# Kernel tuning notes

Measured on AMD Instinct MI355X. Metric: run time of the kernel, lower is better.

Reference implementation:

```python
import jax, jax.numpy as jnp
import numpy as np

N_USERS, N_MOVIES, H, E = 100000, 50000, 128, 1000000


def setup_inputs() -> dict:
    key = jax.random.key(0)
    k1, k2, k3, k4, k5, k6 = jax.random.split(key, 6)
    scale1 = 1.0 / np.sqrt(2 * H)  # torch Linear default-ish init scale
    scale2 = 1.0 / np.sqrt(H)
    return {
        "z_user": jax.random.normal(k1, (N_USERS, H), dtype=jnp.float32),
        "z_movie": jax.random.normal(k2, (N_MOVIES, H), dtype=jnp.float32),
        "row": jax.random.randint(k3, (E,), 0, N_USERS, dtype=jnp.int64) if jax.config.jax_enable_x64 else jax.random.randint(k3, (E,), 0, N_USERS, dtype=jnp.int32),
        "col": jax.random.randint(k4, (E,), 0, N_MOVIES, dtype=jnp.int32),
        "W1": jax.random.normal(k5, (H, 2 * H), dtype=jnp.float32) * scale1,
        "b1": jnp.zeros((H,), dtype=jnp.float32),
        "W2": jax.random.normal(k6, (1, H), dtype=jnp.float32) * scale2,
        "b2": jnp.zeros((1,), dtype=jnp.float32),
    }


def reference(z_user, z_movie, row, col, W1, b1, W2, b2):
    zu = z_user[row]            # [E, H] gather
    zm = z_movie[col]           # [E, H] gather
    z = jnp.concatenate([zu, zm], axis=-1)        # [E, 2H]
    h = jax.nn.relu(z @ W1.T + b1)                # [E, H]
    out = h @ W2.T + b2                           # [E, 1]
    return out.reshape(-1)
```

## Files before the change

kernel.cpp:

```cpp
#include <hip/hip_runtime.h>
#include <stdint.h>

typedef __attribute__((ext_vector_type(8))) short bf16x8;
typedef __attribute__((ext_vector_type(8))) char  char8;
typedef __attribute__((ext_vector_type(4))) float f32x4;
typedef __attribute__((ext_vector_type(4))) int   i32x4;

#define SU      (4.5f / 127.0f)
#define INV_SU  (127.0f / 4.5f)

__device__ __forceinline__ unsigned short f2bf(float f) {
    uint32_t u = __builtin_bit_cast(uint32_t, f);
    uint32_t r = (u + 0x7FFFu + ((u >> 16) & 1u)) >> 16;
    return (unsigned short)r;
}

__device__ __forceinline__ float bf2f(unsigned short u) {
    return __builtin_bit_cast(float, (uint32_t)u << 16);
}

__device__ __forceinline__ bf16x8 cvt8(f32x4 a, f32x4 b) {
    bf16x8 v;
#pragma unroll
    for (int i = 0; i < 4; ++i) v[i] = (short)f2bf(a[i]);
#pragma unroll
    for (int i = 0; i < 4; ++i) v[4 + i] = (short)f2bf(b[i]);
    return v;
}

__device__ __forceinline__ unsigned swz256(int n, int kbyte) {
    return ((unsigned)(n * 256 + kbyte)) ^ (unsigned)((n & 7) << 4);
}

__global__ __launch_bounds__(256) void precompute_h1(
    const float* __restrict__ zu, const float* __restrict__ zm,
    const float* __restrict__ W1, const float* __restrict__ b1,
    char* __restrict__ h1u8, char* __restrict__ h1m8,
    int Mu, int Mm, int bu)
{
    __shared__ __align__(16) char Bs[32768];
    const int tid  = threadIdx.x;
    const int wid  = tid >> 6;
    const int lane = tid & 63;
    const int g    = lane >> 4;
    const int lm   = lane & 15;

    const bool isU = (int)blockIdx.x < bu;
    const float* z = isU ? zu : zm;
    char* h1       = isU ? h1u8 : h1m8;
    const int M    = isU ? Mu : Mm;
    const int koff = isU ? 0 : 128;
    const int rbase = (isU ? blockIdx.x : blockIdx.x - bu) * 128 + wid * 32;

#pragma unroll
    for (int it = 0; it < 8; ++it) {
        int c  = it * 256 + tid;
        int n  = c >> 4;
        int kc = c & 15;
        const float* src = W1 + n * 256 + koff + kc * 8;
        f32x4 a = *reinterpret_cast<const f32x4*>(src);
        f32x4 b = *reinterpret_cast<const f32x4*>(src + 4);
        *reinterpret_cast<bf16x8*>(&Bs[swz256(n, kc * 16)]) = cvt8(a, b);
    }
    __syncthreads();

    f32x4 b1q[8];
#pragma unroll
    for (int nt = 0; nt < 8; ++nt) {
        f32x4 t = *reinterpret_cast<const f32x4*>(b1 + nt * 16 + g * 4);
#pragma unroll
        for (int r = 0; r < 4; ++r) b1q[nt][r] = 0.5f * t[r];
    }

    f32x4 acc[2][8];
#pragma unroll
    for (int mt = 0; mt < 2; ++mt)
#pragma unroll
        for (int nt = 0; nt < 8; ++nt) acc[mt][nt] = f32x4{0.f, 0.f, 0.f, 0.f};

#pragma unroll
    for (int ks = 0; ks < 4; ++ks) {
        bf16x8 a[2];
#pragma unroll
        for (int mt = 0; mt < 2; ++mt) {
            int r = rbase + mt * 16 + lm;
            r = r < M ? r : M - 1;
            const float* p = z + (size_t)r * 128 + ks * 32 + g * 8;
            f32x4 x0 = *reinterpret_cast<const f32x4*>(p);
            f32x4 x1 = *reinterpret_cast<const f32x4*>(p + 4);
            a[mt] = cvt8(x0, x1);
        }
        const int kbyte = (ks * 32 + g * 8) * 2;
#pragma unroll
        for (int nt = 0; nt < 8; ++nt) {
            bf16x8 bfr = *reinterpret_cast<const bf16x8*>(&Bs[swz256(nt * 16 + lm, kbyte)]);
#pragma unroll
            for (int mt = 0; mt < 2; ++mt)
                acc[mt][nt] = __builtin_amdgcn_mfma_f32_16x16x32_bf16(
                    bfr, a[mt], acc[mt][nt], 0, 0, 0);
        }
    }

#pragma unroll
    for (int mt = 0; mt < 2; ++mt) {
        const int m = rbase + mt * 16 + lm;
        if (m >= M) continue;
#pragma unroll
        for (int nt = 0; nt < 8; ++nt) {
            uint32_t p = 0;
#pragma unroll
            for (int r = 0; r < 4; ++r) {
                float h  = acc[mt][nt][r] + b1q[nt][r];
                float qf = fmaxf(-127.f, fminf(127.f, __builtin_rintf(h * INV_SU)));
                int   q  = (int)qf;
                p |= (uint32_t)(q & 0xff) << (8 * r);
            }
            *reinterpret_cast<uint32_t*>(h1 + (size_t)m * 128 + nt * 16 + g * 4) = p;
        }
    }
}

__global__ __launch_bounds__(256) void edge_score(
    const char* __restrict__ h1u8, const char* __restrict__ h1m8,
    const int* __restrict__ row, const int* __restrict__ col,
    const float* __restrict__ W2, const float* __restrict__ b2,
    float* __restrict__ out, int nE)
{
    const int tid = blockIdx.x * 256 + threadIdx.x;
    const int g   = tid >> 4;
    const int l   = tid & 15;
    const int e0  = g * 8;
    if (e0 >= nE) return;

    float w2s[8];
    {
        f32x4 c0 = *reinterpret_cast<const f32x4*>(W2 + l * 8);
        f32x4 c1 = *reinterpret_cast<const f32x4*>(W2 + l * 8 + 4);
#pragma unroll
        for (int j = 0; j < 4; ++j) { w2s[j] = c0[j] * SU; w2s[4 + j] = c1[j] * SU; }
    }
    const float b2s = b2[0];

    int ridx[8], cidx[8];
    if (e0 + 8 <= nE) {
        i32x4 r0 = __builtin_nontemporal_load(reinterpret_cast<const i32x4*>(row + e0));
        i32x4 r1 = __builtin_nontemporal_load(reinterpret_cast<const i32x4*>(row + e0 + 4));
        i32x4 c0 = __builtin_nontemporal_load(reinterpret_cast<const i32x4*>(col + e0));
        i32x4 c1 = __builtin_nontemporal_load(reinterpret_cast<const i32x4*>(col + e0 + 4));
#pragma unroll
        for (int j = 0; j < 4; ++j) { ridx[j] = r0[j]; ridx[4 + j] = r1[j]; }
#pragma unroll
        for (int j = 0; j < 4; ++j) { cidx[j] = c0[j]; cidx[4 + j] = c1[j]; }
    } else {
#pragma unroll
        for (int j = 0; j < 8; ++j) {
            int e = e0 + j;
            e = e < nE ? e : nE - 1;
            ridx[j] = row[e];
            cidx[j] = col[e];
        }
    }

    char8 u[8], m[8];
#pragma unroll
    for (int j = 0; j < 8; ++j)
        u[j] = *reinterpret_cast<const char8*>(h1u8 + (size_t)ridx[j] * 128 + l * 8);
#pragma unroll
    for (int j = 0; j < 8; ++j)
        m[j] = *reinterpret_cast<const char8*>(h1m8 + (size_t)cidx[j] * 128 + l * 8);
    __builtin_amdgcn_sched_barrier(0);

    float s[8];
#pragma unroll
    for (int j = 0; j < 8; ++j) {
        float acc = 0.f;
#pragma unroll
        for (int q = 0; q < 8; ++q) {
            int su = (int)u[j][q] + (int)m[j][q];
            su = su > 0 ? su : 0;
            acc = fmaf((float)su, w2s[q], acc);
        }
        acc += __shfl_xor(acc, 1);
        acc += __shfl_xor(acc, 2);
        acc += __shfl_xor(acc, 4);
        acc += __shfl_xor(acc, 8);
        s[j] = acc + b2s;
    }

    float v = 0.f;
#pragma unroll
    for (int j = 0; j < 8; ++j) v = (l == j) ? s[j] : v;
    const int e = e0 + l;
    if (l < 8 && e < nE) __builtin_nontemporal_store(v, out + e);
}

__device__ __forceinline__ unsigned swzB(int n, int kbyte) {
    return ((unsigned)(n * 512 + kbyte)) ^ (unsigned)((n & 7) << 4);
}

__global__ __launch_bounds__(256, 2) void edge_mlp_fallback(
    const float* __restrict__ z_user, const float* __restrict__ z_movie,
    const int* __restrict__ row, const int* __restrict__ col,
    const float* __restrict__ W1, const float* __restrict__ b1,
    const float* __restrict__ W2, const float* __restrict__ b2,
    float* __restrict__ out, int nE, int ntiles)
{
    __shared__ __align__(16) char Bs[65536];
    const int tid  = threadIdx.x;
    const int wid  = tid >> 6;
    const int lane = tid & 63;
    const int g    = lane >> 4;
    const int lm   = lane & 15;

#pragma unroll
    for (int it = 0; it < 16; ++it) {
        int c  = it * 256 + tid;
        int n  = c >> 5;
        int kc = c & 31;
        const float* src = W1 + n * 256 + kc * 8;
        f32x4 a = *reinterpret_cast<const f32x4*>(src);
        f32x4 b = *reinterpret_cast<const f32x4*>(src + 4);
        *reinterpret_cast<bf16x8*>(&Bs[swzB(n, kc * 16)]) = cvt8(a, b);
    }
    __syncthreads();

    float b1v[8], w2v[8];
#pragma unroll
    for (int nt = 0; nt < 8; ++nt) {
        int n = nt * 16 + lm;
        b1v[nt] = b1[n];
        w2v[nt] = W2[n];
    }
    const float b2s = b2[0];

    for (int tile = blockIdx.x; tile < ntiles; tile += gridDim.x) {
        const int ebase = tile * 256 + wid * 64;
        int re[4], ce[4];
#pragma unroll
        for (int mt = 0; mt < 4; ++mt) {
            int e = ebase + mt * 16 + lm;
            e = e < nE ? e : nE - 1;
            re[mt] = row[e];
            ce[mt] = col[e];
        }
        f32x4 acc[4][8];
#pragma unroll
        for (int mt = 0; mt < 4; ++mt)
#pragma unroll
            for (int nt = 0; nt < 8; ++nt) acc[mt][nt] = f32x4{0.f, 0.f, 0.f, 0.f};
#pragma unroll
        for (int half = 0; half < 2; ++half) {
#pragma unroll
            for (int ks = 0; ks < 4; ++ks) {
                bf16x8 a[4];
#pragma unroll
                for (int mt = 0; mt < 4; ++mt) {
                    const float* p = (half ? z_movie + (size_t)ce[mt] * 128
                                           : z_user + (size_t)re[mt] * 128) + ks * 32 + g * 8;
                    f32x4 x0 = *reinterpret_cast<const f32x4*>(p);
                    f32x4 x1 = *reinterpret_cast<const f32x4*>(p + 4);
                    a[mt] = cvt8(x0, x1);
                }
                const int kbyte = (half * 128 + ks * 32 + g * 8) * 2;
#pragma unroll
                for (int nt = 0; nt < 8; ++nt) {
                    bf16x8 bfr = *reinterpret_cast<const bf16x8*>(&Bs[swzB(nt * 16 + lm, kbyte)]);
#pragma unroll
                    for (int mt = 0; mt < 4; ++mt)
                        acc[mt][nt] = __builtin_amdgcn_mfma_f32_16x16x32_bf16(
                            a[mt], bfr, acc[mt][nt], 0, 0, 0);
                }
            }
        }
#pragma unroll
        for (int mt = 0; mt < 4; ++mt) {
#pragma unroll
            for (int r = 0; r < 4; ++r) {
                float s = 0.f;
#pragma unroll
                for (int nt = 0; nt < 8; ++nt)
                    s += fmaxf(acc[mt][nt][r] + b1v[nt], 0.f) * w2v[nt];
                s += __shfl_xor(s, 8);
                s += __shfl_xor(s, 4);
                s += __shfl_xor(s, 2);
                s += __shfl_xor(s, 1);
                if (lm == 0) {
                    int e = ebase + mt * 16 + g * 4 + r;
                    if (e < nE) out[e] = s + b2s;
                }
            }
        }
    }
}

extern "C" void kernel_launch(void* const* d_in, const int* in_sizes, int n_in,
                              void* d_out, int out_size, void* d_ws, size_t ws_size,
                              hipStream_t stream) {
    const float* z_user  = (const float*)d_in[0];
    const float* z_movie = (const float*)d_in[1];
    const int*   row     = (const int*)d_in[2];
    const int*   col     = (const int*)d_in[3];
    const float* W1      = (const float*)d_in[4];
    const float* b1      = (const float*)d_in[5];
    const float* W2      = (const float*)d_in[6];
    const float* b2      = (const float*)d_in[7];
    float*       out     = (float*)d_out;

    const int nE = in_sizes[2];
    const int Mu = in_sizes[0] / 128;
    const int Mm = in_sizes[1] / 128;

    const size_t need = ((size_t)Mu + (size_t)Mm) * 128;

    if (ws_size >= need) {
        char* h1u8 = (char*)d_ws;
        char* h1m8 = h1u8 + (size_t)Mu * 128;

        const int bu = (Mu + 127) / 128;
        const int bm = (Mm + 127) / 128;
        precompute_h1<<<bu + bm, 256, 0, stream>>>(z_user, z_movie, W1, b1,
                                                   h1u8, h1m8, Mu, Mm, bu);

        const int nGroups = (nE + 7) / 8;
        const int blocks  = (nGroups * 16 + 255) / 256;
        edge_score<<<blocks, 256, 0, stream>>>(h1u8, h1m8, row, col,
                                               W2, b2, out, nE);
    } else {
        const int ntiles = (nE + 255) / 256;
        const int grid   = ntiles < 512 ? ntiles : 512;
        edge_mlp_fallback<<<grid, 256, 0, stream>>>(z_user, z_movie, row, col,
                                                    W1, b1, W2, b2, out, nE, ntiles);
    }
}
```

Baseline: 64.58 us.

## Pre-convert W1 to bf16 MFMA fragment layout in a separate kernel

Adds a small kernel that converts W1 to bf16 once, stored in the exact per-lane fragment order the MFMA loop consumes. precompute_h1 then reads B fragments directly from global memory (cached in L2) instead of having every block convert W1 into LDS and synchronise. This removes redundant per-block conversion work and the LDS use and barrier, which may raise occupancy. The cost is an extra kernel launch and global or L2 reads in the inner loop in place of LDS reads.

```diff
diff --git a/kernel.cpp b/kernel.cpp
--- a/kernel.cpp
+++ b/kernel.cpp
@@ -15,10 +15,6 @@
     return (unsigned short)r;
 }
 
-__device__ __forceinline__ float bf2f(unsigned short u) {
-    return __builtin_bit_cast(float, (uint32_t)u << 16);
-}
-
 __device__ __forceinline__ bf16x8 cvt8(f32x4 a, f32x4 b) {
     bf16x8 v;
 #pragma unroll
@@ -28,17 +24,27 @@
     return v;
 }
 
-__device__ __forceinline__ unsigned swz256(int n, int kbyte) {
-    return ((unsigned)(n * 256 + kbyte)) ^ (unsigned)((n & 7) << 4);
+__global__ void w1cvt(const float* __restrict__ W1, unsigned short* __restrict__ w1bf) {
+    const int idx  = blockIdx.x * 256 + threadIdx.x;
+    const int half = idx >> 11;
+    const int rem  = idx & 2047;
+    const int nt   = rem >> 8;
+    const int ks   = (rem >> 6) & 3;
+    const int lane = rem & 63;
+    const int lm   = lane & 15;
+    const int g    = lane >> 4;
+    const float* src = W1 + (nt * 16 + lm) * 256 + half * 128 + ks * 32 + g * 8;
+    f32x4 a = *reinterpret_cast<const f32x4*>(src);
+    f32x4 b = *reinterpret_cast<const f32x4*>(src + 4);
+    *reinterpret_cast<bf16x8*>(w1bf + (size_t)idx * 8) = cvt8(a, b);
 }
 
 __global__ __launch_bounds__(256) void precompute_h1(
     const float* __restrict__ zu, const float* __restrict__ zm,
-    const float* __restrict__ W1, const float* __restrict__ b1,
+    const unsigned short* __restrict__ w1bf, const float* __restrict__ b1,
     char* __restrict__ h1u8, char* __restrict__ h1m8,
     int Mu, int Mm, int bu)
 {
-    __shared__ __align__(16) char Bs[32768];
     const int tid  = threadIdx.x;
     const int wid  = tid >> 6;
     const int lane = tid & 63;
@@ -49,28 +55,8 @@
     const float* z = isU ? zu : zm;
     char* h1       = isU ? h1u8 : h1m8;
     const int M    = isU ? Mu : Mm;
-    const int koff = isU ? 0 : 128;
+    const unsigned short* wb = w1bf + (isU ? 0 : (size_t)2048 * 8);
     const int rbase = (isU ? blockIdx.x : blockIdx.x - bu) * 128 + wid * 32;
-
-#pragma unroll
-    for (int it = 0; it < 8; ++it) {
-        int c  = it * 256 + tid;
-        int n  = c >> 4;
-        int kc = c & 15;
-        const float* src = W1 + n * 256 + koff + kc * 8;
-        f32x4 a = *reinterpret_cast<const f32x4*>(src);
-        f32x4 b = *reinterpret_cast<const f32x4*>(src + 4);
-        *reinterpret_cast<bf16x8*>(&Bs[swz256(n, kc * 16)]) = cvt8(a, b);
-    }
-    __syncthreads();
-
-    f32x4 b1q[8];
-#pragma unroll
-    for (int nt = 0; nt < 8; ++nt) {
-        f32x4 t = *reinterpret_cast<const f32x4*>(b1 + nt * 16 + g * 4);
-#pragma unroll
-        for (int r = 0; r < 4; ++r) b1q[nt][r] = 0.5f * t[r];
-    }
 
     f32x4 acc[2][8];
 #pragma unroll
@@ -90,15 +76,23 @@
             f32x4 x1 = *reinterpret_cast<const f32x4*>(p + 4);
             a[mt] = cvt8(x0, x1);
         }
-        const int kbyte = (ks * 32 + g * 8) * 2;
 #pragma unroll
         for (int nt = 0; nt < 8; ++nt) {
-            bf16x8 bfr = *reinterpret_cast<const bf16x8*>(&Bs[swz256(nt * 16 + lm, kbyte)]);
+            bf16x8 bfr = *reinterpret_cast<const bf16x8*>(
+                wb + ((size_t)(nt * 4 + ks) * 64 + lane) * 8);
 #pragma unroll
             for (int mt = 0; mt < 2; ++mt)
                 acc[mt][nt] = __builtin_amdgcn_mfma_f32_16x16x32_bf16(
                     bfr, a[mt], acc[mt][nt], 0, 0, 0);
         }
+    }
+
+    f32x4 b1q[8];
+#pragma unroll
+    for (int nt = 0; nt < 8; ++nt) {
+        f32x4 t = *reinterpret_cast<const f32x4*>(b1 + nt * 16 + g * 4);
+#pragma unroll
+        for (int r = 0; r < 4; ++r) b1q[nt][r] = 0.5f * t[r];
     }
 
 #pragma unroll
@@ -310,15 +304,19 @@
     const int Mu = in_sizes[0] / 128;
     const int Mm = in_sizes[1] / 128;
 
-    const size_t need = ((size_t)Mu + (size_t)Mm) * 128;
+    const size_t tblBytes = ((size_t)Mu + (size_t)Mm) * 128;
+    const size_t need     = tblBytes + 65536;
 
     if (ws_size >= need) {
         char* h1u8 = (char*)d_ws;
         char* h1m8 = h1u8 + (size_t)Mu * 128;
+        unsigned short* w1bf = (unsigned short*)(h1u8 + tblBytes);
+
+        w1cvt<<<16, 256, 0, stream>>>(W1, w1bf);
 
         const int bu = (Mu + 127) / 128;
         const int bm = (Mm + 127) / 128;
-        precompute_h1<<<bu + bm, 256, 0, stream>>>(z_user, z_movie, W1, b1,
+        precompute_h1<<<bu + bm, 256, 0, stream>>>(z_user, z_movie, w1bf, b1,
                                                    h1u8, h1m8, Mu, Mm, bu);
 
         const int nGroups = (nE + 7) / 8;
```

Measured after the change: 71.80 us. 11.2% more time.
